# Performance work log

Hardware: AMD Instinct MI355X
Metric: run time of the kernel (lower is better)

The kernel has to match this reference:

```python
import jax, jax.numpy as jnp
import numpy as np

B, L, S, STATIC = 32, 512, 37, 8
D, DI, N, K, DTR, NL, V = 768, 1536, 16, 4, 48, 4, 32


def _rmsnorm(h, w, eps=1e-5):
    var = jnp.mean(h * h, axis=-1, keepdims=True)
    return h * jax.lax.rsqrt(var + eps) * w


def _layernorm(h, w, b, eps=1e-5):
    mu = jnp.mean(h, axis=-1, keepdims=True)
    var = jnp.mean((h - mu) ** 2, axis=-1, keepdims=True)
    return (h - mu) * jax.lax.rsqrt(var + eps) * w + b


def _selective_scan(u, dt, A, Bm, Cm):
    # u, dt: [B,L,Di]; A: [Di,N]; Bm, Cm: [B,L,N]
    def step(h, inp):
        u_t, dt_t, B_t, C_t = inp              # [B,Di],[B,Di],[B,N],[B,N]
        dA = jnp.exp(dt_t[..., None] * A)      # [B,Di,N]
        h = dA * h + (dt_t * u_t)[..., None] * B_t[:, None, :]
        y = jnp.einsum('bdn,bn->bd', h, C_t)
        return h, y
    h0 = jnp.zeros((u.shape[0], DI, N), u.dtype)
    xs = (u.transpose(1, 0, 2), dt.transpose(1, 0, 2),
          Bm.transpose(1, 0, 2), Cm.transpose(1, 0, 2))
    _, ys = jax.lax.scan(step, h0, xs)
    return ys.transpose(1, 0, 2)  # [B,L,Di]


def setup_inputs() -> dict:
    key = jax.random.key(0)
    ks = jax.random.split(key, 24)
    s = 0.02
    inp = {
        'x': jax.random.normal(ks[0], (B, L, S), jnp.float32),
        'static': jax.random.normal(ks[1], (B, STATIC), jnp.float32),
        'time': jax.random.uniform(ks[2], (B, L), jnp.float32),
        'sensor_mask': jax.random.randint(ks[3], (B, L, S), 0, 2, jnp.int32),
        'labels': jax.random.randint(ks[4], (B, L), 0, V, jnp.int64),
        # CEHR embedding params
        'emb_w': jax.random.normal(ks[5], (D, 2 * S), jnp.float32) * s,
        'emb_b': jnp.zeros((D,), jnp.float32),
        'static_w': jax.random.normal(ks[6], (D, STATIC), jnp.float32) * s,
        'static_b': jnp.zeros((D,), jnp.float32),
        'ln_w': jnp.ones((D,), jnp.float32),
        'ln_b': jnp.zeros((D,), jnp.float32),
        # Mamba layers (stacked)
        'norm_w': jnp.ones((NL, D), jnp.float32),
        'in_proj_w': jax.random.normal(ks[7], (NL, 2 * DI, D), jnp.float32) * s,
        'conv_w': jax.random.normal(ks[8], (NL, DI, K), jnp.float32) * s,
        'conv_b': jnp.zeros((NL, DI), jnp.float32),
        'x_proj_w': jax.random.normal(ks[9], (NL, DTR + 2 * N, DI), jnp.float32) * s,
        'dt_proj_w': jax.random.normal(ks[10], (NL, DI, DTR), jnp.float32) * s,
        'dt_proj_b': jnp.full((NL, DI), -4.6, jnp.float32),  # softplus^-1(~0.01)
        'A_log': jnp.broadcast_to(jnp.log(jnp.arange(1, N + 1, dtype=jnp.float32)), (NL, DI, N)).copy(),
        'D_param': jnp.ones((NL, DI), jnp.float32),
        'out_proj_w': jax.random.normal(ks[11], (NL, D, DI), jnp.float32) * s,
        'norm_f_w': jnp.ones((D,), jnp.float32),
        'lm_head_w': jax.random.normal(ks[12], (V, D), jnp.float32) * s,
    }
    return inp


def reference(x, static, time, sensor_mask, labels, emb_w, emb_b, static_w,
              static_b, ln_w, ln_b, norm_w, in_proj_w, conv_w, conv_b,
              x_proj_w, dt_proj_w, dt_proj_b, A_log, D_param, out_proj_w,
              norm_f_w, lm_head_w):
    # ---- CEHR embedding: concat(values, mask) -> D, plus static broadcast ----
    feats = jnp.concatenate([x, sensor_mask.astype(x.dtype)], axis=-1)  # [B,L,2S]
    h = jnp.einsum('blf,df->bld', feats, emb_w) + emb_b
    h = h + (static @ static_w.T + static_b)[:, None, :]
    h = _layernorm(h, ln_w, ln_b)  # [B,L,D]

    # ---- Mamba backbone ----
    for l in range(NL):
        resid = h
        hn = _rmsnorm(h, norm_w[l])
        xz = jnp.einsum('bld,ed->ble', hn, in_proj_w[l])  # [B,L,2*Di]
        xb, z = jnp.split(xz, 2, axis=-1)
        # causal depthwise conv1d, kernel K
        xp = jnp.pad(xb, ((0, 0), (K - 1, 0), (0, 0)))
        xc = sum(conv_w[l][:, k] * xp[:, k:k + L, :] for k in range(K)) + conv_b[l]
        xc = jax.nn.silu(xc)
        proj = jnp.einsum('bld,ed->ble', xc, x_proj_w[l])  # [B,L,DTR+2N]
        dt_r = proj[..., :DTR]
        Bm = proj[..., DTR:DTR + N]
        Cm = proj[..., DTR + N:]
        dt = jax.nn.softplus(jnp.einsum('blr,dr->bld', dt_r, dt_proj_w[l]) + dt_proj_b[l])
        A = -jnp.exp(A_log[l])  # [Di,N]
        y = _selective_scan(xc, dt, A, Bm, Cm) + D_param[l] * xc
        y = y * jax.nn.silu(z)
        h = resid + jnp.einsum('ble,de->bld', y, out_proj_w[l])

    h = _rmsnorm(h, norm_f_w)
    logits = jnp.einsum('bld,vd->blv', h, lm_head_w)  # [B,L,V]
    return logits
```

## Files before the change

kernel.cpp:

```cpp
#include <hip/hip_runtime.h>
#include <math.h>

#define B_ 32
#define L_ 512
#define S_ 37
#define STATIC_ 8
#define D_ 768
#define DI_ 1536
#define N_ 16
#define DTR_ 48
#define NL_ 4
#define V_ 32
#define ROWS_ (B_*L_)
#define CB_ 8
#define CROWS_ (CB_*L_)
#define NCH_ (B_/CB_)
#define KE_ 96
#define TCH_ 64
#define NCHT_ (L_/TCH_)
#define TP4_ 68
#define KS_ 4
#define KSL_ (DI_/KS_)

typedef __bf16 bf16;
typedef __bf16 bf16x8 __attribute__((ext_vector_type(8)));
typedef __bf16 bf16x4 __attribute__((ext_vector_type(4)));
typedef __bf16 bf16x2 __attribute__((ext_vector_type(2)));
typedef float f32x4 __attribute__((ext_vector_type(4)));

typedef __attribute__((address_space(3))) void lds_void;
typedef __attribute__((address_space(1))) const void gmem_void;

__device__ __forceinline__ void gld16(const void* g, void* l) {
    __builtin_amdgcn_global_load_lds((gmem_void*)g, (lds_void*)l, 16, 0, 0);
}

__device__ __forceinline__ float silu_(float x) { return x / (1.f + __expf(-x)); }
__device__ __forceinline__ float softplus_(float x) {
    return fmaxf(x, 0.f) + __logf(1.f + __expf(-fabsf(x)));
}
__device__ __forceinline__ unsigned pack_bf2_(float a, float b) {
    bf16x2 v{(bf16)a, (bf16)b};
    return __builtin_bit_cast(unsigned, v);
}
template<int CTRL>
__device__ __forceinline__ float dpp_add_(float p) {
    int vi = __builtin_amdgcn_update_dpp(0, __builtin_bit_cast(int, p),
                                         CTRL, 0xF, 0xF, true);
    return p + __builtin_bit_cast(float, vi);
}

template<int MODE>
__global__ __launch_bounds__(256) void gemm_mfma(
    const bf16* __restrict__ A, const bf16* __restrict__ W,
    const float* __restrict__ addsrc, void* __restrict__ Cv,
    int Nstore, int K, int ntn,
    const float* __restrict__ dt_bias, unsigned* __restrict__ swg,
    float* __restrict__ pbuf, const bf16* __restrict__ uref)
{
    __shared__ bf16 As[128 * 32];
    __shared__ bf16 Bs[128 * 32];
    const int tid = threadIdx.x;

    int m0, n0, kbeg, kend;
    if (MODE == 4) {
        m0 = blockIdx.y * 128; n0 = 0;
        kbeg = blockIdx.x * KSL_; kend = kbeg + KSL_;
    } else {
        int bid = blockIdx.x;
        int xcd = bid & 7, slot = bid >> 3;
        int Mtiles = gridDim.x / ntn;
        int mband = Mtiles >> 3;
        int m_tile = xcd * mband + slot / ntn;
        int n_tile = slot % ntn;
        m0 = m_tile * 128; n0 = n_tile * 128;
        kbeg = 0; kend = K;
    }

    f32x4 acc[4][4];
    #pragma unroll
    for (int i = 0; i < 4; i++)
        #pragma unroll
        for (int j = 0; j < 4; j++)
            acc[i][j] = f32x4{0.f, 0.f, 0.f, 0.f};

    const int srow = tid >> 2, spart = tid & 3;
    const bf16* ag = A + (size_t)(m0 + srow) * K + spart * 8;
    const bf16* wg = W + (size_t)(n0 + srow) * K + spart * 8;
    char* lA = (char*)As + tid * 16;
    char* lB = (char*)Bs + tid * 16;

    const int lane = tid & 63, wv = tid >> 6;
    const int wr = wv >> 1, wc = wv & 1;
    const int colL = lane & 15, quad = lane >> 4;
    const bf16* aRd = As + (wr * 64 + colL) * 32 + quad * 8;
    const bf16* bRd = Bs + (wc * 64 + colL) * 32 + quad * 8;

    for (int kt = kbeg; kt < kend; kt += 32) {
        gld16(ag + kt, lA);
        gld16(ag + kt + (size_t)64 * K, lA + 4096);
        gld16(wg + kt, lB);
        gld16(wg + kt + (size_t)64 * K, lB + 4096);
        __syncthreads();
        bf16x8 fa[4], fb[4];
        #pragma unroll
        for (int i = 0; i < 4; i++) fa[i] = *(const bf16x8*)(aRd + i * 16 * 32);
        #pragma unroll
        for (int j = 0; j < 4; j++) fb[j] = *(const bf16x8*)(bRd + j * 16 * 32);
        #pragma unroll
        for (int i = 0; i < 4; i++)
            #pragma unroll
            for (int j = 0; j < 4; j++)
                acc[i][j] = __builtin_amdgcn_mfma_f32_16x16x32_bf16(fa[i], fb[j], acc[i][j], 0, 0, 0);
        __syncthreads();
    }

    float* Cf = (float*)Cv;
    bf16*  Cb = (bf16*)Cv;
    #pragma unroll
    for (int i = 0; i < 4; i++) {
        #pragma unroll
        for (int j = 0; j < 4; j++) {
            int n = n0 + wc * 64 + j * 16 + colL;
            #pragma unroll
            for (int r = 0; r < 4; r++) {
                int m = m0 + wr * 64 + i * 16 + quad * 4 + r;
                float v = acc[i][j][r];
                if (MODE == 2) {
                    float dtv = softplus_(v + dt_bias[n]);
                    float u = (float)uref[(size_t)m * DI_ + n];
                    swg[(size_t)m * DI_ + n] = pack_bf2_(dtv * u, dtv);
                } else if (MODE == 4) {
                    if (n < 96)
                        pbuf[((size_t)blockIdx.x * CROWS_ + m) * 96 + n] = v;
                } else if (n < Nstore) {
                    if (addsrc) v += addsrc[(size_t)m * Nstore + n];
                    if (MODE == 1) Cb[(size_t)m * Nstore + n] = (bf16)v;
                    else           Cf[(size_t)m * Nstore + n] = v;
                }
            }
        }
    }
}

__global__ __launch_bounds__(256) void xpost_kernel(const float* __restrict__ pbuf,
                                                    bf16* __restrict__ dtr,
                                                    bf16* __restrict__ bcb) {
    int idx = blockIdx.x * 256 + threadIdx.x;
    int m = idx / 96, j = idx % 96;
    float s = pbuf[idx];
    #pragma unroll
    for (int k = 1; k < KS_; k++) s += pbuf[(size_t)k * CROWS_ * 96 + idx];
    if (j < 64) {
        dtr[(size_t)m * 64 + j] = (bf16)s;
    } else {
        int jj = j - 64;
        int n = jj & 15, hi = jj >> 4;
        bcb[(size_t)m * 32 + 2 * n + hi] = (bf16)s;
    }
}

__global__ __launch_bounds__(256) void cast_f2b_kernel(const float* __restrict__ s,
                                                       bf16* __restrict__ d) {
    size_t i = (size_t)blockIdx.x * 256 + threadIdx.x;
    d[i] = (bf16)s[i];
}

__global__ __launch_bounds__(256) void pad_lm_kernel(const float* __restrict__ s, bf16* __restrict__ d) {
    int i = blockIdx.x * 256 + threadIdx.x;
    int row = i / D_;
    d[i] = (row < V_) ? (bf16)s[i] : (bf16)0.f;
}

__global__ __launch_bounds__(256) void pad_embw_kernel(const float* __restrict__ s, bf16* __restrict__ d) {
    int i = blockIdx.x * 256 + threadIdx.x;
    int row = i / KE_, col = i % KE_;
    d[i] = (col < 2 * S_) ? (bf16)s[row * 2 * S_ + col] : (bf16)0.f;
}

__global__ __launch_bounds__(256) void feats_kernel(const float* __restrict__ x,
                                                    const int* __restrict__ mask,
                                                    bf16* __restrict__ d) {
    size_t i = (size_t)blockIdx.x * 256 + threadIdx.x;
    size_t row = i / KE_;
    int col = (int)(i % KE_);
    float v = 0.f;
    if (col < S_) v = x[row * S_ + col];
    else if (col < 2 * S_) v = (float)mask[row * S_ + (col - S_)];
    d[i] = (bf16)v;
}

__global__ __launch_bounds__(256) void xpw_pad_kernel(const float* __restrict__ xpw,
                                                      bf16* __restrict__ d) {
    int l = blockIdx.y;
    int idx = blockIdx.x * 256 + threadIdx.x;
    int row = idx / DI_, col = idx % DI_;
    float v = 0.f;
    if (row < DTR_) v = xpw[((size_t)l * (DTR_ + 2 * N_) + row) * DI_ + col];
    else if (row >= 64 && row < 96) v = xpw[((size_t)l * (DTR_ + 2 * N_) + row - 16) * DI_ + col];
    d[(size_t)l * 128 * DI_ + idx] = (bf16)v;
}

__global__ __launch_bounds__(256) void dtw_pad_kernel(const float* __restrict__ dtw,
                                                      bf16* __restrict__ d) {
    int l = blockIdx.y;
    int idx = blockIdx.x * 256 + threadIdx.x;
    int row = idx / 64, c = idx % 64;
    float v = (c < DTR_) ? dtw[((size_t)l * DI_ + row) * DTR_ + c] : 0.f;
    d[(size_t)l * DI_ * 64 + idx] = (bf16)v;
}

__global__ __launch_bounds__(256) void sstat_kernel(const float* __restrict__ stat,
                                                    const float* __restrict__ static_w,
                                                    const float* __restrict__ static_b,
                                                    const float* __restrict__ emb_b,
                                                    float* __restrict__ sstat) {
    int i = blockIdx.x * 256 + threadIdx.x;
    int d = i % D_, b = i / D_;
    float acc = emb_b[d] + static_b[d];
    const float* sw = static_w + (size_t)d * STATIC_;
    const float* sv = stat + (size_t)b * STATIC_;
    #pragma unroll
    for (int s = 0; s < STATIC_; s++) acc += sv[s] * sw[s];
    sstat[i] = acc;
}

__device__ __forceinline__ void block_reduce2_(float& a, float& b, float* sbuf) {
    #pragma unroll
    for (int off = 32; off > 0; off >>= 1) {
        a += __shfl_down(a, off, 64);
        b += __shfl_down(b, off, 64);
    }
    int lane = threadIdx.x & 63, wid = threadIdx.x >> 6;
    if (lane == 0) { sbuf[wid] = a; sbuf[4 + wid] = b; }
    __syncthreads();
    a = sbuf[0] + sbuf[1] + sbuf[2] + sbuf[3];
    b = sbuf[4] + sbuf[5] + sbuf[6] + sbuf[7];
}

__global__ __launch_bounds__(256) void ln_embed_kernel(const float* __restrict__ h_pre,
                                                       const float* __restrict__ sstat,
                                                       const float* __restrict__ ln_w,
                                                       const float* __restrict__ ln_b,
                                                       float* __restrict__ h) {
    int row = blockIdx.x, b = row / L_, tid = threadIdx.x;
    __shared__ float sbuf[8];
    float v[3], sum = 0.f, sq = 0.f;
    #pragma unroll
    for (int j = 0; j < 3; j++) {
        int d = tid + 256 * j;
        v[j] = h_pre[(size_t)row * D_ + d] + sstat[b * D_ + d];
        sum += v[j]; sq += v[j] * v[j];
    }
    block_reduce2_(sum, sq, sbuf);
    float mu = sum * (1.f / D_);
    float rstd = rsqrtf(sq * (1.f / D_) - mu * mu + 1e-5f);
    #pragma unroll
    for (int j = 0; j < 3; j++) {
        int d = tid + 256 * j;
        h[(size_t)row * D_ + d] = (v[j] - mu) * rstd * ln_w[d] + ln_b[d];
    }
}

__global__ __launch_bounds__(256) void rmsnorm_bf_kernel(const float* __restrict__ h,
                                                         const float* __restrict__ w,
                                                         bf16* __restrict__ out) {
    int row = blockIdx.x, tid = threadIdx.x;
    __shared__ float sbuf[8];
    float v[3], ss = 0.f, dummy = 0.f;
    #pragma unroll
    for (int j = 0; j < 3; j++) {
        v[j] = h[(size_t)row * D_ + tid + 256 * j];
        ss += v[j] * v[j];
    }
    block_reduce2_(ss, dummy, sbuf);
    float rstd = rsqrtf(ss * (1.f / D_) + 1e-5f);
    #pragma unroll
    for (int j = 0; j < 3; j++) {
        int d = tid + 256 * j;
        out[(size_t)row * D_ + d] = (bf16)(v[j] * rstd * w[d]);
    }
}

__global__ __launch_bounds__(256) void conv_silu_kernel(const bf16* __restrict__ xzb,
                                                        const float* __restrict__ cw,
                                                        const float* __restrict__ cb,
                                                        const float* __restrict__ Dp,
                                                        bf16* __restrict__ xcb,
                                                        unsigned* __restrict__ gag) {
    size_t idx = (size_t)blockIdx.x * 256 + threadIdx.x;
    int d4 = (int)(idx % (DI_ / 4));
    size_t row = idx / (DI_ / 4);
    int t = (int)(row % L_);
    int d = d4 * 4;
    const uint2* xz64 = (const uint2*)xzb;
    size_t base = row * 768 + d4;
    uint2 z2{0u, 0u};
    uint2 p0  = xz64[base];
    uint2 pm1 = (t >= 1) ? xz64[base - 768]     : z2;
    uint2 pm2 = (t >= 2) ? xz64[base - 2 * 768] : z2;
    uint2 pm3 = (t >= 3) ? xz64[base - 3 * 768] : z2;
    uint2 pz  = xz64[base + 384];

    bf16x4 a0 = __builtin_bit_cast(bf16x4, p0);
    bf16x4 a1 = __builtin_bit_cast(bf16x4, pm1);
    bf16x4 a2 = __builtin_bit_cast(bf16x4, pm2);
    bf16x4 a3 = __builtin_bit_cast(bf16x4, pm3);
    bf16x4 az = __builtin_bit_cast(bf16x4, pz);

    float cbl[4], Dl[4];
    *(float4*)cbl = ((const float4*)cb)[d4];
    *(float4*)Dl  = ((const float4*)Dp)[d4];

    float u[4];
    unsigned gv[4];
    #pragma unroll
    for (int c = 0; c < 4; c++) {
        float4 wc = ((const float4*)cw)[d + c];
        float acc = cbl[c] + wc.x * (float)a3[c] + wc.y * (float)a2[c]
                           + wc.z * (float)a1[c] + wc.w * (float)a0[c];
        u[c] = silu_(acc);
        float gz = silu_((float)az[c]);
        gv[c] = pack_bf2_(Dl[c] * u[c] * gz, gz);
    }
    ((uint2*)xcb)[row * (DI_ / 4) + d4] = uint2{pack_bf2_(u[0], u[1]), pack_bf2_(u[2], u[3])};
    *(uint4*)(gag + row * DI_ + d) = uint4{gv[0], gv[1], gv[2], gv[3]};
}

__global__ __launch_bounds__(256) void scan_lds_kernel(const unsigned* __restrict__ bcp,
                                                       const unsigned* __restrict__ swg,
                                                       const unsigned* __restrict__ gag,
                                                       const float* __restrict__ A_log,
                                                       bf16* __restrict__ yb) {
    __shared__ unsigned lsw[2][16][TP4_];
    __shared__ unsigned lga[2][16][TP4_];
    __shared__ unsigned lbc[2][16][TP4_];
    const int tid = threadIdx.x;
    const int n = tid & 15, dl = tid >> 4;
    const int d = blockIdx.x * 16 + dl;
    const int b = blockIdx.y;
    const float AvL = -__expf(A_log[(size_t)d * N_ + n]) * 1.44269504f;
    const size_t seqbase = (size_t)b * L_;
    const int d0 = blockIdx.x * 16;

    unsigned swr[4], gar[4], bcr[4];

    #define GLOAD(c)                                                        \
        {                                                                   \
            size_t rb = seqbase + (size_t)(c) * TCH_;                       \
            _Pragma("unroll")                                               \
            for (int i = 0; i < 4; i++) {                                   \
                size_t g = rb + i * 16 + dl;                                \
                swr[i] = swg[g * DI_ + d0 + n];                             \
                gar[i] = gag[g * DI_ + d0 + n];                             \
                bcr[i] = bcp[g * 16 + n];                                   \
            }                                                               \
        }
    #define DSWRITE(p)                                                      \
        {                                                                   \
            _Pragma("unroll")                                               \
            for (int i = 0; i < 4; i++) {                                   \
                int t = i * 16 + dl;                                        \
                lsw[p][n][t] = swr[i];                                      \
                lga[p][n][t] = gar[i];                                      \
                lbc[p][n][t] = bcr[i];                                      \
            }                                                               \
        }

    GLOAD(0);
    DSWRITE(0);
    __syncthreads();
    GLOAD(1);

    float h = 0.f;
    for (int c = 0; c < NCHT_; c++) {
        int p = c & 1;
        bf16* py = yb + (seqbase + (size_t)c * TCH_) * DI_ + d;
        #pragma unroll 4
        for (int t0 = 0; t0 < TCH_; t0 += 4) {
            uint4 s4 = *(const uint4*)&lsw[p][dl][t0];
            uint4 b4 = *(const uint4*)&lbc[p][n][t0];
            uint4 g4{0u, 0u, 0u, 0u};
            if (n == 0) g4 = *(const uint4*)&lga[p][dl][t0];
            unsigned ss[4] = {s4.x, s4.y, s4.z, s4.w};
            unsigned bb[4] = {b4.x, b4.y, b4.z, b4.w};
            unsigned gg[4] = {g4.x, g4.y, g4.z, g4.w};
            #pragma unroll
            for (int u = 0; u < 4; u++) {
                bf16x2 dv = __builtin_bit_cast(bf16x2, ss[u]);
                bf16x2 bcv = __builtin_bit_cast(bf16x2, bb[u]);
                float du = (float)dv.x, dtv = (float)dv.y;
                float dA = __builtin_amdgcn_exp2f(dtv * AvL);
                h = dA * h + du * (float)bcv.x;
                float pq = h * (float)bcv.y;
                pq = dpp_add_<0xB1>(pq);
                pq = dpp_add_<0x4E>(pq);
                pq = dpp_add_<0x124>(pq);
                pq = dpp_add_<0x128>(pq);
                if (n == 0) {
                    bf16x2 og = __builtin_bit_cast(bf16x2, gg[u]);
                    py[(size_t)(t0 + u) * DI_] = (bf16)(pq * (float)og.y + (float)og.x);
                }
            }
        }
        if (c + 1 < NCHT_) {
            DSWRITE(p ^ 1);
            __syncthreads();
            if (c + 2 < NCHT_) GLOAD(c + 2);
        }
    }
    #undef GLOAD
    #undef DSWRITE
}

extern "C" void kernel_launch(void* const* d_in, const int* in_sizes, int n_in,
                              void* d_out, int out_size, void* d_ws, size_t ws_size,
                              hipStream_t stream) {
    const float* x        = (const float*)d_in[0];
    const float* stat     = (const float*)d_in[1];
    const int*   mask     = (const int*)d_in[3];
    const float* emb_w    = (const float*)d_in[5];
    const float* emb_b    = (const float*)d_in[6];
    const float* static_w = (const float*)d_in[7];
    const float* static_b = (const float*)d_in[8];
    const float* ln_w     = (const float*)d_in[9];
    const float* ln_b     = (const float*)d_in[10];
    const float* norm_w   = (const float*)d_in[11];
    const float* in_proj_w  = (const float*)d_in[12];
    const float* conv_w   = (const float*)d_in[13];
    const float* conv_b   = (const float*)d_in[14];
    const float* x_proj_w = (const float*)d_in[15];
    const float* dt_proj_w= (const float*)d_in[16];
    const float* dt_proj_b= (const float*)d_in[17];
    const float* A_log    = (const float*)d_in[18];
    const float* D_param  = (const float*)d_in[19];
    const float* out_proj_w = (const float*)d_in[20];
    const float* norm_f_w = (const float*)d_in[21];
    const float* lm_head_w= (const float*)d_in[22];
    float* out = (float*)d_out;

    char* p = (char*)d_ws;
    float*    h      = (float*)p;         p += (size_t)ROWS_ * D_ * 4;
    bf16*     hn_bf  = (bf16*)p;          p += (size_t)CROWS_ * D_ * 2;
    char*     xz_region = p;
    bf16*     xz_bf  = (bf16*)p;          p += (size_t)CROWS_ * 2 * DI_ * 2;
    bf16*     xc_bf  = (bf16*)p;          p += (size_t)CROWS_ * DI_ * 2;
    unsigned* sw_g   = (unsigned*)p;      p += (size_t)CROWS_ * DI_ * 4;
    unsigned* gate_g = (unsigned*)p;      p += (size_t)CROWS_ * DI_ * 4;
    bf16*     bc16   = (bf16*)p;          p += (size_t)CROWS_ * 32 * 2;
    bf16*     dtr_bf = (bf16*)p;          p += (size_t)CROWS_ * 64 * 2;
    float*    pbuf   = (float*)p;         p += (size_t)KS_ * CROWS_ * 96 * 4;
    bf16*     y_bf   = (bf16*)p;          p += (size_t)ROWS_ * DI_ * 2;
    bf16*     inw_l  = (bf16*)p;          p += (size_t)2 * DI_ * D_ * 2;
    bf16*     outw_l = (bf16*)p;          p += (size_t)D_ * DI_ * 2;
    bf16*     xpwp_bf= (bf16*)p;          p += (size_t)NL_ * 128 * DI_ * 2;
    bf16*     dtwp_bf= (bf16*)p;          p += (size_t)NL_ * DI_ * 64 * 2;
    bf16*     lmw_bf = (bf16*)p;          p += (size_t)128 * D_ * 2;
    bf16*     embw_bf= (bf16*)p;          p += (size_t)D_ * KE_ * 2;
    bf16*     feats  = (bf16*)p;          p += (size_t)ROWS_ * KE_ * 2;
    float*    sstat  = (float*)p;         p += (size_t)B_ * D_ * 4;
    float*    h_pre  = (float*)xz_region;
    bf16*     hn_full= (bf16*)sw_g;

    pad_lm_kernel<<<(128 * D_) / 256, 256, 0, stream>>>(lm_head_w, lmw_bf);
    pad_embw_kernel<<<(D_ * KE_) / 256, 256, 0, stream>>>(emb_w, embw_bf);
    feats_kernel<<<(ROWS_ * KE_) / 256, 256, 0, stream>>>(x, mask, feats);
    dim3 gxp((128 * DI_) / 256, NL_);
    xpw_pad_kernel<<<gxp, 256, 0, stream>>>(x_proj_w, xpwp_bf);
    dim3 gdt((DI_ * 64) / 256, NL_);
    dtw_pad_kernel<<<gdt, 256, 0, stream>>>(dt_proj_w, dtwp_bf);
    sstat_kernel<<<(B_ * D_) / 256, 256, 0, stream>>>(stat, static_w, static_b, emb_b, sstat);

    gemm_mfma<0><<<(D_ / 128) * (ROWS_ / 128), 256, 0, stream>>>(
        feats, embw_bf, nullptr, h_pre, D_, KE_, D_ / 128,
        nullptr, nullptr, nullptr, nullptr);
    ln_embed_kernel<<<ROWS_, 256, 0, stream>>>(h_pre, sstat, ln_w, ln_b, h);

    for (int l = 0; l < NL_; l++) {
        cast_f2b_kernel<<<(2 * DI_ * D_) / 256, 256, 0, stream>>>(
            in_proj_w + (size_t)l * 2 * DI_ * D_, inw_l);
        cast_f2b_kernel<<<(D_ * DI_) / 256, 256, 0, stream>>>(
            out_proj_w + (size_t)l * D_ * DI_, outw_l);

        for (int c = 0; c < NCH_; c++) {
            float* hc = h + (size_t)c * CROWS_ * D_;

            rmsnorm_bf_kernel<<<CROWS_, 256, 0, stream>>>(hc, norm_w + (size_t)l * D_, hn_bf);

            gemm_mfma<1><<<(2 * DI_ / 128) * (CROWS_ / 128), 256, 0, stream>>>(
                hn_bf, inw_l, nullptr, xz_bf, 2 * DI_, D_, 2 * DI_ / 128,
                nullptr, nullptr, nullptr, nullptr);

            conv_silu_kernel<<<(CROWS_ * DI_ / 4) / 256, 256, 0, stream>>>(
                xz_bf, conv_w + (size_t)l * DI_ * 4, conv_b + (size_t)l * DI_,
                D_param + (size_t)l * DI_, xc_bf, gate_g);

            dim3 g2a(KS_, CROWS_ / 128);
            gemm_mfma<4><<<g2a, 256, 0, stream>>>(xc_bf, xpwp_bf + (size_t)l * 128 * DI_,
                                                  nullptr, nullptr, 0, DI_, 1,
                                                  nullptr, nullptr, pbuf, nullptr);
            xpost_kernel<<<(CROWS_ * 96) / 256, 256, 0, stream>>>(pbuf, dtr_bf, bc16);

            gemm_mfma<2><<<(DI_ / 128) * (CROWS_ / 128), 256, 0, stream>>>(
                dtr_bf, dtwp_bf + (size_t)l * DI_ * 64, nullptr, nullptr, 0, 64, DI_ / 128,
                dt_proj_b + (size_t)l * DI_, sw_g, nullptr, xc_bf);

            dim3 gs(DI_ / 16, CB_);
            scan_lds_kernel<<<gs, 256, 0, stream>>>((const unsigned*)bc16, sw_g, gate_g,
                                                    A_log + (size_t)l * DI_ * N_,
                                                    y_bf + (size_t)c * CROWS_ * DI_);
        }

        gemm_mfma<0><<<(D_ / 128) * (ROWS_ / 128), 256, 0, stream>>>(
            y_bf, outw_l, h, h, D_, DI_, D_ / 128,
            nullptr, nullptr, nullptr, nullptr);
    }

    rmsnorm_bf_kernel<<<ROWS_, 256, 0, stream>>>(h, norm_f_w, hn_full);
    gemm_mfma<0><<<ROWS_ / 128, 256, 0, stream>>>(
        hn_full, lmw_bf, nullptr, out, V_, D_, 1,
        nullptr, nullptr, nullptr, nullptr);
}
```

Baseline: 2.915 ms.

## Add 256x256-tile pipelined MFMA GEMM for in_proj and out_proj

Adds a new GEMM kernel that uses 256x256 output tiles with 512 threads. It double-buffers LDS through direct global-to-LDS loads with XOR swizzling and interleaves staging with MFMA phases, using setprio and barriers. It also remaps block IDs to group work across XCDs. The in-projection and out-projection GEMMs now use it, aiming for more operand reuse and for hiding global-load latency. In exchange it uses 128KB of LDS and a large accumulator register footprint, and it launches fewer blocks on the smaller per-chunk GEMM.

```diff
diff --git a/kernel.cpp b/kernel.cpp
--- a/kernel.cpp
+++ b/kernel.cpp
@@ -141,6 +141,147 @@
             }
         }
     }
+}
+
+template<int MODE>
+__global__ __launch_bounds__(512, 2) void gemm256(
+    const bf16* __restrict__ A, const bf16* __restrict__ W,
+    const float* __restrict__ addsrc, void* __restrict__ Cv,
+    int Nstore, int K, int ntn)
+{
+    __shared__ bf16 lds[65536];
+    const int tid = threadIdx.x;
+
+    const int bid = blockIdx.x;
+    const int qx = gridDim.x >> 3;
+    const int wgid = (bid & 7) * qx + (bid >> 3);
+    const int m0 = (wgid / ntn) * 256;
+    const int n0 = (wgid % ntn) * 256;
+
+    const int r0 = tid >> 3;
+    const int scol = ((tid & 7) * 8) ^ ((r0 & 7) << 3);
+    const size_t sK = (size_t)K;
+    const bf16* aSrc = A + (size_t)(m0 + r0) * sK + scol;
+    const bf16* bSrc = W + (size_t)(n0 + r0) * sK + scol;
+    char* ldst = (char*)lds + tid * 16;
+
+#define STAGE_A(h, t) { const bf16* s_ = aSrc + (size_t)(h) * 128 * sK + (t) * 64;   \
+    char* d_ = ldst + ((t) & 1) * 65536 + (h) * 16384;                               \
+    gld16(s_, d_); gld16(s_ + 64 * sK, d_ + 8192); }
+#define STAGE_B(h, t) { const bf16* s_ = bSrc + (size_t)(h) * 128 * sK + (t) * 64;   \
+    char* d_ = ldst + ((t) & 1) * 65536 + 32768 + (h) * 16384;                       \
+    gld16(s_, d_); gld16(s_ + 64 * sK, d_ + 8192); }
+
+    const int lane = tid & 63, w = tid >> 6;
+    const int wr = w >> 2, wc = w & 3;
+    const int colL = lane & 15, quad = lane >> 4;
+    const int sx = (colL & 7) << 3;
+    const int c0 = (quad * 8) ^ sx;
+    const int c1 = c0 ^ 32;
+    const bf16* aRd0 = lds + wr * 8192 + colL * 64 + c0;
+    const bf16* aRd1 = lds + wr * 8192 + colL * 64 + c1;
+    const bf16* bRd0 = lds + 16384 + (wc >> 1) * 8192 + ((wc & 1) * 64 + colL) * 64 + c0;
+    const bf16* bRd1 = lds + 16384 + (wc >> 1) * 8192 + ((wc & 1) * 64 + colL) * 64 + c1;
+
+    f32x4 acc[8][4];
+    #pragma unroll
+    for (int i = 0; i < 8; i++)
+        #pragma unroll
+        for (int j = 0; j < 4; j++)
+            acc[i][j] = f32x4{0.f, 0.f, 0.f, 0.f};
+    bf16x8 aF[4][2], bF[4][2];
+
+#define RD_A(buf, mp) { _Pragma("unroll") for (int i = 0; i < 4; i++) {              \
+    aF[i][0] = *(const bf16x8*)(aRd0 + (buf) * 32768 + (mp) * 4096 + i * 1024);      \
+    aF[i][1] = *(const bf16x8*)(aRd1 + (buf) * 32768 + (mp) * 4096 + i * 1024); } }
+#define RD_B01(buf) { _Pragma("unroll") for (int j = 0; j < 2; j++) {                \
+    bF[j][0] = *(const bf16x8*)(bRd0 + (buf) * 32768 + j * 1024);                    \
+    bF[j][1] = *(const bf16x8*)(bRd1 + (buf) * 32768 + j * 1024); } }
+#define RD_B23(buf) { _Pragma("unroll") for (int j = 0; j < 2; j++) {                \
+    bF[2 + j][0] = *(const bf16x8*)(bRd0 + (buf) * 32768 + (2 + j) * 1024);          \
+    bF[2 + j][1] = *(const bf16x8*)(bRd1 + (buf) * 32768 + (2 + j) * 1024); } }
+#define MM(mp, np) { _Pragma("unroll") for (int i = 0; i < 4; i++)                   \
+    _Pragma("unroll") for (int j = 0; j < 2; j++) {                                  \
+    acc[(mp)*4+i][(np)*2+j] = __builtin_amdgcn_mfma_f32_16x16x32_bf16(               \
+        aF[i][0], bF[(np)*2+j][0], acc[(mp)*4+i][(np)*2+j], 0, 0, 0);                \
+    acc[(mp)*4+i][(np)*2+j] = __builtin_amdgcn_mfma_f32_16x16x32_bf16(               \
+        aF[i][1], bF[(np)*2+j][1], acc[(mp)*4+i][(np)*2+j], 0, 0, 0); } }
+#define MID_SYNC  __builtin_amdgcn_s_barrier();                                      \
+    asm volatile("s_waitcnt lgkmcnt(0)" ::: "memory");                               \
+    __builtin_amdgcn_sched_barrier(0);                                               \
+    __builtin_amdgcn_s_setprio(1);
+#define END_PHASE __builtin_amdgcn_s_setprio(0); __builtin_amdgcn_s_barrier();
+
+    const int NT = K >> 6;
+    const int NI = NT >> 1;
+
+    STAGE_B(0, 0); STAGE_B(1, 0); STAGE_A(0, 0); STAGE_A(1, 0);
+    STAGE_B(0, 1); STAGE_B(1, 1);
+    asm volatile("s_waitcnt vmcnt(4)" ::: "memory");
+    __builtin_amdgcn_s_barrier();
+
+    for (int it = 0; it < NI; ++it) {
+        const int t0 = 2 * it, t1 = t0 + 1;
+        const bool nlast = (it + 1 < NI);
+        RD_A(0, 0); RD_B01(0);
+        STAGE_A(0, t1);
+        MID_SYNC; MM(0, 0); END_PHASE;
+        RD_B23(0);
+        STAGE_A(1, t1);
+        MID_SYNC; MM(0, 1); END_PHASE;
+        RD_A(0, 1);
+        if (nlast) STAGE_B(0, t0 + 2);
+        MID_SYNC; MM(1, 0); END_PHASE;
+        if (nlast) STAGE_B(1, t0 + 2);
+        MID_SYNC; MM(1, 1);
+        __builtin_amdgcn_s_setprio(0);
+        if (nlast) { asm volatile("s_waitcnt vmcnt(4)" ::: "memory"); }
+        else       { asm volatile("s_waitcnt vmcnt(0)" ::: "memory"); }
+        __builtin_amdgcn_s_barrier();
+        RD_A(1, 0); RD_B01(1);
+        if (nlast) STAGE_A(0, t0 + 2);
+        MID_SYNC; MM(0, 0); END_PHASE;
+        RD_B23(1);
+        if (nlast) STAGE_A(1, t0 + 2);
+        MID_SYNC; MM(0, 1); END_PHASE;
+        RD_A(1, 1);
+        if (nlast) STAGE_B(0, t1 + 2);
+        MID_SYNC; MM(1, 0); END_PHASE;
+        if (nlast) STAGE_B(1, t1 + 2);
+        MID_SYNC; MM(1, 1);
+        __builtin_amdgcn_s_setprio(0);
+        if (nlast) { asm volatile("s_waitcnt vmcnt(4)" ::: "memory"); }
+        __builtin_amdgcn_s_barrier();
+    }
+
+    float* Cf = (float*)Cv;
+    bf16*  Cb = (bf16*)Cv;
+    #pragma unroll
+    for (int f = 0; f < 8; f++) {
+        #pragma unroll
+        for (int j = 0; j < 4; j++) {
+            int n = n0 + wc * 64 + j * 16 + colL;
+            #pragma unroll
+            for (int r = 0; r < 4; r++) {
+                int m = m0 + wr * 128 + f * 16 + quad * 4 + r;
+                float v = acc[f][j][r];
+                if (MODE == 0) {
+                    v += addsrc[(size_t)m * Nstore + n];
+                    Cf[(size_t)m * Nstore + n] = v;
+                } else {
+                    Cb[(size_t)m * Nstore + n] = (bf16)v;
+                }
+            }
+        }
+    }
+#undef STAGE_A
+#undef STAGE_B
+#undef RD_A
+#undef RD_B01
+#undef RD_B23
+#undef MM
+#undef MID_SYNC
+#undef END_PHASE
 }
 
 __global__ __launch_bounds__(256) void xpost_kernel(const float* __restrict__ pbuf,
@@ -487,9 +628,8 @@
 
             rmsnorm_bf_kernel<<<CROWS_, 256, 0, stream>>>(hc, norm_w + (size_t)l * D_, hn_bf);
 
-            gemm_mfma<1><<<(2 * DI_ / 128) * (CROWS_ / 128), 256, 0, stream>>>(
-                hn_bf, inw_l, nullptr, xz_bf, 2 * DI_, D_, 2 * DI_ / 128,
-                nullptr, nullptr, nullptr, nullptr);
+            gemm256<1><<<(CROWS_ / 256) * (2 * DI_ / 256), 512, 0, stream>>>(
+                hn_bf, inw_l, nullptr, xz_bf, 2 * DI_, D_, 2 * DI_ / 256);
 
             conv_silu_kernel<<<(CROWS_ * DI_ / 4) / 256, 256, 0, stream>>>(
                 xz_bf, conv_w + (size_t)l * DI_ * 4, conv_b + (size_t)l * DI_,
@@ -511,9 +651,8 @@
                                                     y_bf + (size_t)c * CROWS_ * DI_);
         }
 
-        gemm_mfma<0><<<(D_ / 128) * (ROWS_ / 128), 256, 0, stream>>>(
-            y_bf, outw_l, h, h, D_, DI_, D_ / 128,
-            nullptr, nullptr, nullptr, nullptr);
+        gemm256<0><<<(ROWS_ / 256) * (D_ / 256), 512, 0, stream>>>(
+            y_bf, outw_l, h, h, D_, DI_, D_ / 256);
     }
 
     rmsnorm_bf_kernel<<<ROWS_, 256, 0, stream>>>(h, norm_f_w, hn_full);
```

Result: faster. 2.740 ms (-6.0%).
